# Optimization experiments

Hardware: AMD Instinct MI355X
Metric: run time of the kernel (lower is better)

## Reference

```python
import jax, jax.numpy as jnp
import numpy as np

B, T, N, U = 16, 512, 2048, 64  # batch_size, dim1, dim2 (=nodes), units


def setup_inputs() -> dict:
    key = jax.random.key(0)
    k1, k2, k3, k4 = jax.random.split(key, 4)
    x = jax.random.normal(k1, (B, T, N), dtype=jnp.float32)
    Adj = jax.random.uniform(k2, (N, N), dtype=jnp.float32)
    W = jax.random.normal(k3, (U, N), dtype=jnp.float32) * 0.05  # 'uniform' init stand-in
    b = jax.random.normal(k4, (U,), dtype=jnp.float32) * 0.05
    return {"x": x, "Adj": Adj, "W": W, "b": b}


def reference(x, Adj, W, b):
    # Original loop: out_i[b,t,j] = sum_k x[b,t,k] * Adj[j,k] * W[i,k] + b[i],
    # then mean over i. By linearity this equals a single matmul with the
    # unit-averaged weight vector and the averaged bias.
    w_bar = jnp.mean(W, axis=0)              # [N]
    w_eff = Adj * w_bar                       # [N(j), N(k)] : Adj[j,k] * w_bar[k]
    out = jnp.einsum('btk,jk->btj', x, w_eff) + jnp.mean(b)
    return out  # [B, T, N]
```

## Files before the change

kernel.cpp:

```cpp
#include <hip/hip_runtime.h>

#define N_DIM 2048
#define U_DIM 64
#define M_DIM 8192
#define K_DIM 2048

typedef __bf16 bf16x8 __attribute__((ext_vector_type(8)));
typedef float  floatx4 __attribute__((ext_vector_type(4)));
typedef unsigned short ushort8 __attribute__((ext_vector_type(8)));

#define AS1 __attribute__((address_space(1)))
#define AS3 __attribute__((address_space(3)))

__device__ __forceinline__ unsigned short f_to_bf16_rne(float f) {
    unsigned int x;
    __builtin_memcpy(&x, &f, 4);
    x += 0x7fffu + ((x >> 16) & 1u);
    return (unsigned short)(x >> 16);
}

__global__ __launch_bounds__(256) void prep_kernel(
    const float* __restrict__ W, const float* __restrict__ b,
    float* __restrict__ wbar, float* __restrict__ bmean) {
    int k = blockIdx.x * 256 + threadIdx.x;
    float s = 0.f;
#pragma unroll
    for (int i = 0; i < U_DIM; ++i) s += W[i * N_DIM + k];
    wbar[k] = s * (1.f / U_DIM);

    if (blockIdx.x == 0 && threadIdx.x < 64) {
        float v = b[threadIdx.x];
#pragma unroll
        for (int off = 32; off > 0; off >>= 1) v += __shfl_down(v, off);
        if (threadIdx.x == 0) bmean[0] = v * (1.f / U_DIM);
    }
}

__global__ __launch_bounds__(256) void weff_kernel(
    const float* __restrict__ Adj, const float* __restrict__ wbar,
    unsigned short* __restrict__ weff) {
    long long idx = ((long long)blockIdx.x * 256 + threadIdx.x) * 8;
    int k = (int)(idx & (N_DIM - 1));
    floatx4 a0 = *(const floatx4*)(Adj + idx);
    floatx4 a1 = *(const floatx4*)(Adj + idx + 4);
    floatx4 w0 = *(const floatx4*)(wbar + k);
    floatx4 w1 = *(const floatx4*)(wbar + k + 4);
    ushort8 ov;
#pragma unroll
    for (int j = 0; j < 4; ++j) {
        ov[j]     = f_to_bf16_rne(a0[j] * w0[j]);
        ov[j + 4] = f_to_bf16_rne(a1[j] * w1[j]);
    }
    *(ushort8*)(weff + idx) = ov;
}

__global__ __launch_bounds__(256) void convx_kernel(
    const float* __restrict__ x, unsigned short* __restrict__ xbf) {
    long long idx = ((long long)blockIdx.x * 256 + threadIdx.x) * 8;
    floatx4 a0 = *(const floatx4*)(x + idx);
    floatx4 a1 = *(const floatx4*)(x + idx + 4);
    ushort8 ov;
#pragma unroll
    for (int j = 0; j < 4; ++j) {
        ov[j]     = f_to_bf16_rne(a0[j]);
        ov[j + 4] = f_to_bf16_rne(a1[j]);
    }
    *(ushort8*)(xbf + idx) = ov;
}

#define BM 128
#define BN 128
#define BK 64

__global__ __launch_bounds__(256) void gemm_bt_kernel(
    const unsigned short* __restrict__ A,
    const unsigned short* __restrict__ Bt,
    const float* __restrict__ bmeanp,
    float* __restrict__ C) {
    __shared__ __align__(16) unsigned short sA[BM * BK];
    __shared__ __align__(16) unsigned short sB[BN * BK];

    const int tid  = threadIdx.x;
    const int w    = tid >> 6;
    const int lane = tid & 63;
    const int tile_m = blockIdx.y * BM;
    const int tile_n = blockIdx.x * BN;

    const float bmean = bmeanp[0];

    const int srow_in = lane >> 3;
    const int skc     = (lane & 7) ^ srow_in;
    const int scol    = skc * 8;
    const unsigned short* gA[4];
    const unsigned short* gB[4];
    unsigned short* lA[4];
    unsigned short* lB[4];
#pragma unroll
    for (int i = 0; i < 4; ++i) {
        int c = w * 4 + i;
        gA[i] = A  + (size_t)(tile_m + c * 8 + srow_in) * K_DIM + scol;
        gB[i] = Bt + (size_t)(tile_n + c * 8 + srow_in) * K_DIM + scol;
        lA[i] = &sA[c * 8 * BK];
        lB[i] = &sB[c * 8 * BK];
    }

    const int wrow = (w >> 1) * 64;
    const int wcol = (w & 1) * 64;
    const int fr = lane & 15;
    const int fq = lane >> 4;
    int aoff[4][2], boff[4][2];
#pragma unroll
    for (int i = 0; i < 4; ++i)
#pragma unroll
        for (int s = 0; s < 2; ++s) {
            int kc = s * 4 + fq;
            int slot = kc ^ (fr & 7);
            aoff[i][s] = (wrow + i * 16 + fr) * BK + slot * 8;
            boff[i][s] = (wcol + i * 16 + fr) * BK + slot * 8;
        }

    floatx4 acc[4][4];
#pragma unroll
    for (int mi = 0; mi < 4; ++mi)
#pragma unroll
        for (int ni = 0; ni < 4; ++ni) acc[mi][ni] = (floatx4){0.f, 0.f, 0.f, 0.f};

    for (int k0 = 0; k0 < K_DIM; k0 += BK) {
        __syncthreads();
#pragma unroll
        for (int i = 0; i < 4; ++i) {
            __builtin_amdgcn_global_load_lds((const AS1 void*)(gA[i] + k0),
                                             (AS3 void*)lA[i], 16, 0, 0);
            __builtin_amdgcn_global_load_lds((const AS1 void*)(gB[i] + k0),
                                             (AS3 void*)lB[i], 16, 0, 0);
        }
        __syncthreads();

#pragma unroll
        for (int s = 0; s < 2; ++s) {
            bf16x8 af[4], bf[4];
#pragma unroll
            for (int i = 0; i < 4; ++i) {
                af[i] = *(const bf16x8*)&sA[aoff[i][s]];
                bf[i] = *(const bf16x8*)&sB[boff[i][s]];
            }
#pragma unroll
            for (int mi = 0; mi < 4; ++mi)
#pragma unroll
                for (int ni = 0; ni < 4; ++ni)
                    acc[mi][ni] = __builtin_amdgcn_mfma_f32_16x16x32_bf16(
                        af[mi], bf[ni], acc[mi][ni], 0, 0, 0);
        }
    }

    const int crow = tile_m + wrow + fq * 4;
    const int ccol = tile_n + wcol + fr;
#pragma unroll
    for (int mi = 0; mi < 4; ++mi)
#pragma unroll
        for (int ni = 0; ni < 4; ++ni)
#pragma unroll
            for (int r = 0; r < 4; ++r) {
                int gm = crow + mi * 16 + r;
                int gn = ccol + ni * 16;
                C[(size_t)gm * N_DIM + gn] = acc[mi][ni][r] + bmean;
            }
}

extern "C" void kernel_launch(void* const* d_in, const int* in_sizes, int n_in,
                              void* d_out, int out_size, void* d_ws, size_t ws_size,
                              hipStream_t stream) {
    (void)in_sizes; (void)n_in; (void)out_size;
    const float* x   = (const float*)d_in[0];
    const float* Adj = (const float*)d_in[1];
    const float* W   = (const float*)d_in[2];
    const float* b   = (const float*)d_in[3];
    float* out = (float*)d_out;

    char* ws = (char*)d_ws;
    float* wbar  = (float*)ws;
    float* bmean = (float*)(ws + 8192);
    unsigned short* weff = (unsigned short*)(ws + 16384);
    const size_t weff_bytes = (size_t)N_DIM * N_DIM * 2;
    const size_t xbf_off = 16384 + weff_bytes;
    unsigned short* xbf = (unsigned short*)(ws + xbf_off);

    size_t avail = (ws_size > xbf_off) ? (ws_size - xbf_off) : 0;
    long long max_rows = (long long)(avail / ((size_t)K_DIM * 2)) / BM * BM;
    if (max_rows < BM) max_rows = BM;
    if (max_rows > M_DIM) max_rows = M_DIM;

    prep_kernel<<<N_DIM / 256, 256, 0, stream>>>(W, b, wbar, bmean);
    weff_kernel<<<(int)(((size_t)N_DIM * N_DIM / 8) / 256), 256, 0, stream>>>(Adj, wbar, weff);

    for (long long m0 = 0; m0 < M_DIM; m0 += max_rows) {
        long long rows = (M_DIM - m0 < max_rows) ? (M_DIM - m0) : max_rows;
        convx_kernel<<<(int)rows, 256, 0, stream>>>(x + m0 * K_DIM, xbf);
        dim3 grid(N_DIM / BN, (int)(rows / BM));
        gemm_bt_kernel<<<grid, 256, 0, stream>>>(xbf, weff, bmean, out + m0 * (size_t)N_DIM);
    }
}
```

Before: 226.7 us.

## Fuse weight and input bf16 conversion kernels and remap GEMM tiles per XCD

Merges the Adj*w_bar bf16 conversion and the x bf16 conversion into one launch when the workspace fits all rows, removing a kernel launch and its serialization. The GEMM grid becomes 1D, with tile indices remapped so each XCD (block id mod 8) gets a fixed pair of N tiles. The aim is better L2 reuse of weff columns within each XCD. The chunked fallback path keeps separate launches and never uses the mtiles argument. The remap assumes block ids are dispatched round-robin across 8 XCDs.

```diff
diff --git a/kernel.cpp b/kernel.cpp
--- a/kernel.cpp
+++ b/kernel.cpp
@@ -36,22 +36,36 @@
     }
 }
 
-__global__ __launch_bounds__(256) void weff_kernel(
+__global__ __launch_bounds__(256) void weff_convx_kernel(
     const float* __restrict__ Adj, const float* __restrict__ wbar,
-    unsigned short* __restrict__ weff) {
-    long long idx = ((long long)blockIdx.x * 256 + threadIdx.x) * 8;
-    int k = (int)(idx & (N_DIM - 1));
-    floatx4 a0 = *(const floatx4*)(Adj + idx);
-    floatx4 a1 = *(const floatx4*)(Adj + idx + 4);
-    floatx4 w0 = *(const floatx4*)(wbar + k);
-    floatx4 w1 = *(const floatx4*)(wbar + k + 4);
-    ushort8 ov;
-#pragma unroll
-    for (int j = 0; j < 4; ++j) {
-        ov[j]     = f_to_bf16_rne(a0[j] * w0[j]);
-        ov[j + 4] = f_to_bf16_rne(a1[j] * w1[j]);
-    }
-    *(ushort8*)(weff + idx) = ov;
+    unsigned short* __restrict__ weff,
+    const float* __restrict__ x, unsigned short* __restrict__ xbf) {
+    if (blockIdx.x < 2048) {
+        long long idx = ((long long)blockIdx.x * 256 + threadIdx.x) * 8;
+        int k = (int)(idx & (N_DIM - 1));
+        floatx4 a0 = *(const floatx4*)(Adj + idx);
+        floatx4 a1 = *(const floatx4*)(Adj + idx + 4);
+        floatx4 w0 = *(const floatx4*)(wbar + k);
+        floatx4 w1 = *(const floatx4*)(wbar + k + 4);
+        ushort8 ov;
+#pragma unroll
+        for (int j = 0; j < 4; ++j) {
+            ov[j]     = f_to_bf16_rne(a0[j] * w0[j]);
+            ov[j + 4] = f_to_bf16_rne(a1[j] * w1[j]);
+        }
+        *(ushort8*)(weff + idx) = ov;
+    } else {
+        long long idx = ((long long)(blockIdx.x - 2048) * 256 + threadIdx.x) * 8;
+        floatx4 a0 = *(const floatx4*)(x + idx);
+        floatx4 a1 = *(const floatx4*)(x + idx + 4);
+        ushort8 ov;
+#pragma unroll
+        for (int j = 0; j < 4; ++j) {
+            ov[j]     = f_to_bf16_rne(a0[j]);
+            ov[j + 4] = f_to_bf16_rne(a1[j]);
+        }
+        *(ushort8*)(xbf + idx) = ov;
+    }
 }
 
 __global__ __launch_bounds__(256) void convx_kernel(
@@ -76,15 +90,22 @@
     const unsigned short* __restrict__ A,
     const unsigned short* __restrict__ Bt,
     const float* __restrict__ bmeanp,
-    float* __restrict__ C) {
+    float* __restrict__ C,
+    int mtiles) {
     __shared__ __align__(16) unsigned short sA[BM * BK];
     __shared__ __align__(16) unsigned short sB[BN * BK];
+
+    const int id    = blockIdx.x;
+    const int xcd   = id & 7;
+    const int local = id >> 3;
+    const int nt    = xcd * 2 + (local & 1);
+    const int mt    = local >> 1;
+    const int tile_m = mt * BM;
+    const int tile_n = nt * BN;
 
     const int tid  = threadIdx.x;
     const int w    = tid >> 6;
     const int lane = tid & 63;
-    const int tile_m = blockIdx.y * BM;
-    const int tile_n = blockIdx.x * BN;
 
     const float bmean = bmeanp[0];
 
@@ -165,6 +186,7 @@
                 int gn = ccol + ni * 16;
                 C[(size_t)gm * N_DIM + gn] = acc[mi][ni][r] + bmean;
             }
+    (void)mtiles;
 }
 
 extern "C" void kernel_launch(void* const* d_in, const int* in_sizes, int n_in,
@@ -191,12 +213,18 @@
     if (max_rows > M_DIM) max_rows = M_DIM;
 
     prep_kernel<<<N_DIM / 256, 256, 0, stream>>>(W, b, wbar, bmean);
-    weff_kernel<<<(int)(((size_t)N_DIM * N_DIM / 8) / 256), 256, 0, stream>>>(Adj, wbar, weff);
-
-    for (long long m0 = 0; m0 < M_DIM; m0 += max_rows) {
-        long long rows = (M_DIM - m0 < max_rows) ? (M_DIM - m0) : max_rows;
-        convx_kernel<<<(int)rows, 256, 0, stream>>>(x + m0 * K_DIM, xbf);
-        dim3 grid(N_DIM / BN, (int)(rows / BM));
-        gemm_bt_kernel<<<grid, 256, 0, stream>>>(xbf, weff, bmean, out + m0 * (size_t)N_DIM);
-    }
-}
+
+    if (max_rows == M_DIM) {
+        weff_convx_kernel<<<2048 + M_DIM, 256, 0, stream>>>(Adj, wbar, weff, x, xbf);
+        gemm_bt_kernel<<<(N_DIM / BN) * (M_DIM / BM), 256, 0, stream>>>(
+            xbf, weff, bmean, out, M_DIM / BM);
+    } else {
+        weff_convx_kernel<<<2048, 256, 0, stream>>>(Adj, wbar, weff, x, xbf);
+        for (long long m0 = 0; m0 < M_DIM; m0 += max_rows) {
+            long long rows = (M_DIM - m0 < max_rows) ? (M_DIM - m0) : max_rows;
+            convx_kernel<<<(int)rows, 256, 0, stream>>>(x + m0 * K_DIM, xbf);
+            gemm_bt_kernel<<<(N_DIM / BN) * (int)(rows / BM), 256, 0, stream>>>(
+                xbf, weff, bmean, out + m0 * (size_t)N_DIM, (int)(rows / BM));
+        }
+    }
+}
```

Result: no change. 226.4 us (median of 2 runs) (-0.1%).

## Fuse fp32-to-bf16 conversion of x into GEMM A-tile loading with XCD-aware tile mapping

Applied to the files above, without the earlier changes.

Removes the separate convx kernel and its bf16 staging buffer. The GEMM now loads fp32 x directly into registers, converts pairs with the packed bf16 intrinsic, and writes them to LDS. The next K-slab is prefetched into registers while MFMAs run. It also switches to a 1D grid that maps neighbouring blocks to the same XCD for N-tile locality. This saves the extra write and read of a 32MB intermediate and a kernel launch, but doubles A global traffic per tile (fp32) and adds register pressure and VALU conversion work inside the main loop.

```diff
diff --git a/kernel.cpp b/kernel.cpp
--- a/kernel.cpp
+++ b/kernel.cpp
@@ -1,4 +1,5 @@
 #include <hip/hip_runtime.h>
+#include <hip/hip_bf16.h>
 
 #define N_DIM 2048
 #define U_DIM 64
@@ -7,6 +8,7 @@
 
 typedef __bf16 bf16x8 __attribute__((ext_vector_type(8)));
 typedef float  floatx4 __attribute__((ext_vector_type(4)));
+typedef unsigned int   uintx4  __attribute__((ext_vector_type(4)));
 typedef unsigned short ushort8 __attribute__((ext_vector_type(8)));
 
 #define AS1 __attribute__((address_space(1)))
@@ -17,6 +19,13 @@
     __builtin_memcpy(&x, &f, 4);
     x += 0x7fffu + ((x >> 16) & 1u);
     return (unsigned short)(x >> 16);
+}
+
+__device__ __forceinline__ unsigned int cvt2_bf16(float lo, float hi) {
+    __hip_bfloat162 h = __float22bfloat162_rn(make_float2(lo, hi));
+    unsigned int u;
+    __builtin_memcpy(&u, &h, 4);
+    return u;
 }
 
 __global__ __launch_bounds__(256) void prep_kernel(
@@ -54,54 +63,46 @@
     *(ushort8*)(weff + idx) = ov;
 }
 
-__global__ __launch_bounds__(256) void convx_kernel(
-    const float* __restrict__ x, unsigned short* __restrict__ xbf) {
-    long long idx = ((long long)blockIdx.x * 256 + threadIdx.x) * 8;
-    floatx4 a0 = *(const floatx4*)(x + idx);
-    floatx4 a1 = *(const floatx4*)(x + idx + 4);
-    ushort8 ov;
-#pragma unroll
-    for (int j = 0; j < 4; ++j) {
-        ov[j]     = f_to_bf16_rne(a0[j]);
-        ov[j + 4] = f_to_bf16_rne(a1[j]);
-    }
-    *(ushort8*)(xbf + idx) = ov;
-}
-
 #define BM 128
 #define BN 128
 #define BK 64
 
-__global__ __launch_bounds__(256) void gemm_bt_kernel(
-    const unsigned short* __restrict__ A,
+__global__ __launch_bounds__(256) void gemm_fused_kernel(
+    const float* __restrict__ X,
     const unsigned short* __restrict__ Bt,
     const float* __restrict__ bmeanp,
     float* __restrict__ C) {
     __shared__ __align__(16) unsigned short sA[BM * BK];
     __shared__ __align__(16) unsigned short sB[BN * BK];
 
+    const int id    = blockIdx.x;
+    const int xcd   = id & 7;
+    const int local = id >> 3;
+    const int nt    = xcd * 2 + (local & 1);
+    const int mt    = local >> 1;
+    const int tile_m = mt * BM;
+    const int tile_n = nt * BN;
+
     const int tid  = threadIdx.x;
     const int w    = tid >> 6;
     const int lane = tid & 63;
-    const int tile_m = blockIdx.y * BM;
-    const int tile_n = blockIdx.x * BN;
 
     const float bmean = bmeanp[0];
 
     const int srow_in = lane >> 3;
     const int skc     = (lane & 7) ^ srow_in;
     const int scol    = skc * 8;
-    const unsigned short* gA[4];
+    const float* gX[4];
     const unsigned short* gB[4];
-    unsigned short* lA[4];
     unsigned short* lB[4];
+    unsigned short* lAw[4];
 #pragma unroll
     for (int i = 0; i < 4; ++i) {
         int c = w * 4 + i;
-        gA[i] = A  + (size_t)(tile_m + c * 8 + srow_in) * K_DIM + scol;
-        gB[i] = Bt + (size_t)(tile_n + c * 8 + srow_in) * K_DIM + scol;
-        lA[i] = &sA[c * 8 * BK];
-        lB[i] = &sB[c * 8 * BK];
+        gX[i]  = X  + (size_t)(tile_m + c * 8 + srow_in) * K_DIM + scol;
+        gB[i]  = Bt + (size_t)(tile_n + c * 8 + srow_in) * K_DIM + scol;
+        lB[i]  = &sB[c * 8 * BK];
+        lAw[i] = &sA[c * 8 * BK] + (size_t)lane * 8;
     }
 
     const int wrow = (w >> 1) * 64;
@@ -125,16 +126,38 @@
 #pragma unroll
         for (int ni = 0; ni < 4; ++ni) acc[mi][ni] = (floatx4){0.f, 0.f, 0.f, 0.f};
 
+    floatx4 ar[4][2];
+#pragma unroll
+    for (int i = 0; i < 4; ++i) {
+        ar[i][0] = *(const floatx4*)(gX[i]);
+        ar[i][1] = *(const floatx4*)(gX[i] + 4);
+    }
+
     for (int k0 = 0; k0 < K_DIM; k0 += BK) {
         __syncthreads();
+
 #pragma unroll
         for (int i = 0; i < 4; ++i) {
-            __builtin_amdgcn_global_load_lds((const AS1 void*)(gA[i] + k0),
-                                             (AS3 void*)lA[i], 16, 0, 0);
+            uintx4 pk;
+            pk[0] = cvt2_bf16(ar[i][0][0], ar[i][0][1]);
+            pk[1] = cvt2_bf16(ar[i][0][2], ar[i][0][3]);
+            pk[2] = cvt2_bf16(ar[i][1][0], ar[i][1][1]);
+            pk[3] = cvt2_bf16(ar[i][1][2], ar[i][1][3]);
+            *(uintx4*)lAw[i] = pk;
+        }
+#pragma unroll
+        for (int i = 0; i < 4; ++i)
             __builtin_amdgcn_global_load_lds((const AS1 void*)(gB[i] + k0),
                                              (AS3 void*)lB[i], 16, 0, 0);
-        }
         __syncthreads();
+
+        if (k0 + BK < K_DIM) {
+#pragma unroll
+            for (int i = 0; i < 4; ++i) {
+                ar[i][0] = *(const floatx4*)(gX[i] + k0 + BK);
+                ar[i][1] = *(const floatx4*)(gX[i] + k0 + BK + 4);
+            }
+        }
 
 #pragma unroll
         for (int s = 0; s < 2; ++s) {
@@ -170,7 +193,7 @@
 extern "C" void kernel_launch(void* const* d_in, const int* in_sizes, int n_in,
                               void* d_out, int out_size, void* d_ws, size_t ws_size,
                               hipStream_t stream) {
-    (void)in_sizes; (void)n_in; (void)out_size;
+    (void)in_sizes; (void)n_in; (void)out_size; (void)ws_size;
     const float* x   = (const float*)d_in[0];
     const float* Adj = (const float*)d_in[1];
     const float* W   = (const float*)d_in[2];
@@ -181,22 +204,10 @@
     float* wbar  = (float*)ws;
     float* bmean = (float*)(ws + 8192);
     unsigned short* weff = (unsigned short*)(ws + 16384);
-    const size_t weff_bytes = (size_t)N_DIM * N_DIM * 2;
-    const size_t xbf_off = 16384 + weff_bytes;
-    unsigned short* xbf = (unsigned short*)(ws + xbf_off);
-
-    size_t avail = (ws_size > xbf_off) ? (ws_size - xbf_off) : 0;
-    long long max_rows = (long long)(avail / ((size_t)K_DIM * 2)) / BM * BM;
-    if (max_rows < BM) max_rows = BM;
-    if (max_rows > M_DIM) max_rows = M_DIM;
 
     prep_kernel<<<N_DIM / 256, 256, 0, stream>>>(W, b, wbar, bmean);
-    weff_kernel<<<(int)(((size_t)N_DIM * N_DIM / 8) / 256), 256, 0, stream>>>(Adj, wbar, weff);
-
-    for (long long m0 = 0; m0 < M_DIM; m0 += max_rows) {
-        long long rows = (M_DIM - m0 < max_rows) ? (M_DIM - m0) : max_rows;
-        convx_kernel<<<(int)rows, 256, 0, stream>>>(x + m0 * K_DIM, xbf);
-        dim3 grid(N_DIM / BN, (int)(rows / BM));
-        gemm_bt_kernel<<<grid, 256, 0, stream>>>(xbf, weff, bmean, out + m0 * (size_t)N_DIM);
-    }
-}
+    weff_kernel<<<(int)(((size_t)N_DIM * N_DIM / 8) / 256), 256, 0, stream>>>(
+        Adj, wbar, weff);
+    gemm_fused_kernel<<<(N_DIM / BN) * (M_DIM / BM), 256, 0, stream>>>(
+        x, weff, bmean, out);
+}
```

Measured after the change: 248.8 us. 1.1x slower.
